# Kernel tuning notes

Measured on AMD Instinct MI355X. Metric: run time of the kernel, lower is better.

The kernel has to match this reference:

```python
import jax, jax.numpy as jnp
import numpy as np

N, E, F_IN, H, OUT, G = 40000, 640000, 128, 128, 10, 256


def setup_inputs() -> dict:
    key = jax.random.key(0)
    ks = jax.random.split(key, 8)
    x = jax.random.normal(ks[0], (N, F_IN), dtype=jnp.float32)
    edge_index = jax.random.randint(ks[1], (2, E), 0, N, dtype=jnp.int32)
    batch = jnp.sort(jax.random.randint(ks[2], (N,), 0, G, dtype=jnp.int32))
    W1 = jax.random.normal(ks[3], (F_IN, H), dtype=jnp.float32) / np.sqrt(F_IN)
    b1 = jnp.zeros((H,), dtype=jnp.float32)
    W2 = jax.random.normal(ks[4], (H, H), dtype=jnp.float32) / np.sqrt(H)
    b2 = jnp.zeros((H,), dtype=jnp.float32)
    Wfc = jax.random.normal(ks[5], (H, OUT), dtype=jnp.float32) / np.sqrt(H)
    bfc = jnp.zeros((OUT,), dtype=jnp.float32)
    return {"x": x, "edge_index": edge_index, "batch": batch,
            "W1": W1, "b1": b1, "W2": W2, "b2": b2, "Wfc": Wfc, "bfc": bfc}


def _gcn_conv(x, W, b, row, col, num_nodes):
    # x' = D^{-1/2} (A+I) D^{-1/2} (x W) + b   (self-loops already in row/col)
    xw = x @ W                                            # [N, H]
    ones = jnp.ones(row.shape[0], dtype=x.dtype)
    deg = jax.ops.segment_sum(ones, col, num_segments=num_nodes)
    dinv = jnp.where(deg > 0, jax.lax.rsqrt(jnp.maximum(deg, 1.0)), 0.0)
    norm = dinv[row] * dinv[col]                          # [E+N]
    msg = xw[row] * norm[:, None]                         # gather + scale
    return jax.ops.segment_sum(msg, col, num_segments=num_nodes) + b


def reference(x, edge_index, batch, W1, b1, W2, b2, Wfc, bfc):
    num_nodes = x.shape[0]
    loop = jnp.arange(num_nodes, dtype=edge_index.dtype)
    row = jnp.concatenate([edge_index[0], loop])
    col = jnp.concatenate([edge_index[1], loop])

    h = jax.nn.relu(_gcn_conv(x, W1, b1, row, col, num_nodes))
    h = jax.nn.relu(_gcn_conv(h, W2, b2, row, col, num_nodes))

    # global_mean_pool over graph ids
    sums = jax.ops.segment_sum(h, batch, num_segments=G)  # [G, H]
    cnt = jax.ops.segment_sum(jnp.ones(num_nodes, h.dtype), batch, num_segments=G)
    pooled = sums / jnp.maximum(cnt, 1.0)[:, None]

    logits = pooled @ Wfc + bfc                           # [G, OUT]
    return jax.nn.log_softmax(logits, axis=-1)
```

## Files before the change

kernel.cpp:

```cpp
#include <hip/hip_runtime.h>
#include <math.h>

#define H_DIM 128
#define OUT_DIM 10

typedef __attribute__((ext_vector_type(8))) __bf16 bf16x8;
typedef __attribute__((ext_vector_type(8))) unsigned short ushort8;
typedef __attribute__((ext_vector_type(4))) float f32x4;

__device__ inline unsigned short f2bf_rne(float f) {
    unsigned int u = __float_as_uint(f);
    unsigned int r = u + 0x7FFFu + ((u >> 16) & 1u);
    return (unsigned short)(r >> 16);
}
__device__ inline float bf_lo(unsigned int u) { return __uint_as_float(u << 16); }
__device__ inline float bf_hi(unsigned int u) { return __uint_as_float(u & 0xFFFF0000u); }

__global__ __launch_bounds__(256) void hist_kernel(const int* __restrict__ col,
                                                   int* __restrict__ cnt, int E) {
    int e = blockIdx.x * 256 + threadIdx.x;
    if (e < E) atomicAdd(&cnt[col[e]], 1);
}

__global__ __launch_bounds__(256) void scan_phase1(const int* __restrict__ cnt,
                                                   int* __restrict__ blockSums,
                                                   float* __restrict__ dinv, int N) {
    __shared__ int red[256];
    int base = blockIdx.x * 1024;
    int t = threadIdx.x;
    int s = 0;
    for (int i = 0; i < 4; ++i) {
        int idx = base + t * 4 + i;
        if (idx < N) {
            int cv = cnt[idx];
            s += cv;
            dinv[idx] = rsqrtf((float)cv + 1.0f);
        }
    }
    red[t] = s;
    __syncthreads();
    for (int d = 128; d > 0; d >>= 1) {
        if (t < d) red[t] += red[t + d];
        __syncthreads();
    }
    if (t == 0) blockSums[blockIdx.x] = red[0];
}

__global__ __launch_bounds__(256) void scan_phase2(const int* __restrict__ blockSums,
                                                   int* __restrict__ blockOffs,
                                                   int* __restrict__ offs, int B, int N) {
    __shared__ int sh[256];
    int t = threadIdx.x;
    sh[t] = (t < B) ? blockSums[t] : 0;
    __syncthreads();
    for (int d = 1; d < 256; d <<= 1) {
        int v = (t >= d) ? sh[t - d] : 0;
        __syncthreads();
        sh[t] += v;
        __syncthreads();
    }
    if (t < B) blockOffs[t] = (t == 0) ? 0 : sh[t - 1];
    if (t == 255) offs[N] = sh[255];
}

__global__ __launch_bounds__(256) void scan_phase3(const int* __restrict__ cnt,
                                                   const int* __restrict__ blockOffs,
                                                   int* __restrict__ offs,
                                                   int* __restrict__ cursor, int N) {
    __shared__ int red[256];
    int base = blockIdx.x * 1024;
    int t = threadIdx.x;
    int v[4];
    int s = 0;
    for (int i = 0; i < 4; ++i) {
        int idx = base + t * 4 + i;
        v[i] = (idx < N) ? cnt[idx] : 0;
        s += v[i];
    }
    red[t] = s;
    __syncthreads();
    for (int d = 1; d < 256; d <<= 1) {
        int x = (t >= d) ? red[t - d] : 0;
        __syncthreads();
        red[t] += x;
        __syncthreads();
    }
    int run = blockOffs[blockIdx.x] + ((t == 0) ? 0 : red[t - 1]);
    for (int i = 0; i < 4; ++i) {
        int idx = base + t * 4 + i;
        if (idx < N) { offs[idx] = run; cursor[idx] = run; run += v[i]; }
    }
}

__global__ __launch_bounds__(256) void scatter_kernel(const int* __restrict__ row,
                                                      const int* __restrict__ col,
                                                      const float* __restrict__ dinv,
                                                      int* __restrict__ cursor,
                                                      int2* __restrict__ csr, int E) {
    int e = blockIdx.x * 256 + threadIdx.x;
    if (e >= E) return;
    int r = row[e], c = col[e];
    int pos = atomicAdd(&cursor[c], 1);
    int2 p; p.x = r; p.y = __float_as_int(dinv[r] * dinv[c]);
    csr[pos] = p;
}

__global__ __launch_bounds__(256) void wconvert(const float* __restrict__ W1,
                                                const float* __restrict__ W2,
                                                unsigned short* __restrict__ Wt1Hi,
                                                unsigned short* __restrict__ Wt1Lo,
                                                unsigned short* __restrict__ Wt2Hi,
                                                unsigned short* __restrict__ Wt2Lo) {
    int i = blockIdx.x * 256 + threadIdx.x;
    const float* src       = (i < 16384) ? W1    : W2;
    unsigned short* dh     = (i < 16384) ? Wt1Hi : Wt2Hi;
    unsigned short* dl     = (i < 16384) ? Wt1Lo : Wt2Lo;
    int idx = i & 16383;
    int k = idx >> 7, n = idx & 127;
    float v = src[idx];
    unsigned short hb = f2bf_rne(v);
    float hf = __uint_as_float((unsigned int)hb << 16);
    unsigned short lb = f2bf_rne(v - hf);
    dh[n * H_DIM + k] = hb;
    dl[n * H_DIM + k] = lb;
}

__global__ __launch_bounds__(256) void xsplit(const float* __restrict__ X,
                                              unsigned short* __restrict__ Xhi,
                                              unsigned short* __restrict__ Xlo,
                                              int total8) {
    int i = blockIdx.x * 256 + threadIdx.x;
    if (i >= total8) return;
    const float* p = X + (size_t)i * 8;
    f32x4 a = *(const f32x4*)p;
    f32x4 b = *(const f32x4*)(p + 4);
    float v[8] = {a.x, a.y, a.z, a.w, b.x, b.y, b.z, b.w};
    ushort8 h, l;
    #pragma unroll
    for (int j = 0; j < 8; ++j) {
        unsigned short hb = f2bf_rne(v[j]);
        float hf = __uint_as_float((unsigned int)hb << 16);
        h[j] = hb;
        l[j] = f2bf_rne(v[j] - hf);
    }
    *(ushort8*)(Xhi + (size_t)i * 8) = h;
    *(ushort8*)(Xlo + (size_t)i * 8) = l;
}

__global__ __launch_bounds__(256) void gemm_mfma_splitA(const unsigned short* __restrict__ Ahi,
                                                        const unsigned short* __restrict__ Alo,
                                                        const unsigned short* __restrict__ WtHi,
                                                        const unsigned short* __restrict__ WtLo,
                                                        unsigned short* __restrict__ Yb, int N) {
    int lane = threadIdx.x & 63;
    int wv   = threadIdx.x >> 6;
    int m16  = lane & 15;
    int quad = lane >> 4;
    int nodeBase = blockIdx.x * 32;

    f32x4 acc[2][2] = {};

    #pragma unroll
    for (int kt = 0; kt < 4; ++kt) {
        int k0 = kt * 32 + quad * 8;

        ushort8 aHi[2], aLo[2];
        #pragma unroll
        for (int mi = 0; mi < 2; ++mi) {
            int node = nodeBase + mi * 16 + m16;
            if (node >= N) node = N - 1;
            size_t off = (size_t)node * H_DIM + k0;
            aHi[mi] = *(const ushort8*)(Ahi + off);
            aLo[mi] = *(const ushort8*)(Alo + off);
        }

        ushort8 bHi[2], bLo[2];
        #pragma unroll
        for (int ni = 0; ni < 2; ++ni) {
            int n = (wv * 2 + ni) * 16 + m16;
            size_t off = (size_t)n * H_DIM + k0;
            bHi[ni] = *(const ushort8*)(WtHi + off);
            bLo[ni] = *(const ushort8*)(WtLo + off);
        }

        #pragma unroll
        for (int mi = 0; mi < 2; ++mi)
            #pragma unroll
            for (int ni = 0; ni < 2; ++ni) {
                acc[mi][ni] = __builtin_amdgcn_mfma_f32_16x16x32_bf16(
                    __builtin_bit_cast(bf16x8, aHi[mi]),
                    __builtin_bit_cast(bf16x8, bHi[ni]), acc[mi][ni], 0, 0, 0);
                acc[mi][ni] = __builtin_amdgcn_mfma_f32_16x16x32_bf16(
                    __builtin_bit_cast(bf16x8, aLo[mi]),
                    __builtin_bit_cast(bf16x8, bHi[ni]), acc[mi][ni], 0, 0, 0);
                acc[mi][ni] = __builtin_amdgcn_mfma_f32_16x16x32_bf16(
                    __builtin_bit_cast(bf16x8, aHi[mi]),
                    __builtin_bit_cast(bf16x8, bLo[ni]), acc[mi][ni], 0, 0, 0);
            }
    }

    #pragma unroll
    for (int mi = 0; mi < 2; ++mi)
        #pragma unroll
        for (int r = 0; r < 4; ++r) {
            int node = nodeBase + mi * 16 + quad * 4 + r;
            if (node < N) {
                #pragma unroll
                for (int ni = 0; ni < 2; ++ni) {
                    int c = (wv * 2 + ni) * 16 + m16;
                    Yb[(size_t)node * H_DIM + c] = f2bf_rne(acc[mi][ni][r]);
                }
            }
        }
}

__global__ __launch_bounds__(256) void gemm_mfma_bf16A(const unsigned short* __restrict__ Xb,
                                                       const unsigned short* __restrict__ WtHi,
                                                       const unsigned short* __restrict__ WtLo,
                                                       unsigned short* __restrict__ Yb, int N) {
    int lane = threadIdx.x & 63;
    int wv   = threadIdx.x >> 6;
    int m16  = lane & 15;
    int quad = lane >> 4;
    int nodeBase = blockIdx.x * 32;

    f32x4 acc[2][2] = {};

    #pragma unroll
    for (int kt = 0; kt < 4; ++kt) {
        int k0 = kt * 32 + quad * 8;

        ushort8 a[2];
        #pragma unroll
        for (int mi = 0; mi < 2; ++mi) {
            int node = nodeBase + mi * 16 + m16;
            if (node >= N) node = N - 1;
            a[mi] = *(const ushort8*)(Xb + (size_t)node * H_DIM + k0);
        }

        ushort8 bHi[2], bLo[2];
        #pragma unroll
        for (int ni = 0; ni < 2; ++ni) {
            int n = (wv * 2 + ni) * 16 + m16;
            size_t off = (size_t)n * H_DIM + k0;
            bHi[ni] = *(const ushort8*)(WtHi + off);
            bLo[ni] = *(const ushort8*)(WtLo + off);
        }

        #pragma unroll
        for (int mi = 0; mi < 2; ++mi)
            #pragma unroll
            for (int ni = 0; ni < 2; ++ni) {
                acc[mi][ni] = __builtin_amdgcn_mfma_f32_16x16x32_bf16(
                    __builtin_bit_cast(bf16x8, a[mi]),
                    __builtin_bit_cast(bf16x8, bHi[ni]), acc[mi][ni], 0, 0, 0);
                acc[mi][ni] = __builtin_amdgcn_mfma_f32_16x16x32_bf16(
                    __builtin_bit_cast(bf16x8, a[mi]),
                    __builtin_bit_cast(bf16x8, bLo[ni]), acc[mi][ni], 0, 0, 0);
            }
    }

    #pragma unroll
    for (int mi = 0; mi < 2; ++mi)
        #pragma unroll
        for (int r = 0; r < 4; ++r) {
            int node = nodeBase + mi * 16 + quad * 4 + r;
            if (node < N) {
                #pragma unroll
                for (int ni = 0; ni < 2; ++ni) {
                    int c = (wv * 2 + ni) * 16 + m16;
                    Yb[(size_t)node * H_DIM + c] = f2bf_rne(acc[mi][ni][r]);
                }
            }
        }
}

__global__ __launch_bounds__(256) void agg_fused(const unsigned short* __restrict__ XWb,
                                                 const float* __restrict__ dinv,
                                                 const int2* __restrict__ csr,
                                                 const int* __restrict__ offs,
                                                 const float* __restrict__ bias,
                                                 unsigned short* __restrict__ OUTb, int N) {
    int wave = (blockIdx.x * 256 + threadIdx.x) >> 6;
    int lane = threadIdx.x & 63;
    if (wave >= N) return;
    int c = wave;
    int start = offs[c], end = offs[c + 1];
    float dc = dinv[c];
    const unsigned int* XW32 = (const unsigned int*)XWb;

    float ax0, ay0;
    {
        unsigned int u = XW32[(size_t)c * 64 + lane];
        float s = dc * dc;
        ax0 = bf_lo(u) * s; ay0 = bf_hi(u) * s;
    }
    float ax1 = 0.f, ay1 = 0.f, ax2 = 0.f, ay2 = 0.f, ax3 = 0.f, ay3 = 0.f;

    for (int base = start; base < end; base += 64) {
        int m = end - base; if (m > 64) m = 64;
        int2 ce; ce.x = 0; ce.y = 0;
        if (lane < m) ce = csr[base + lane];

        int j = 0;
        for (; j + 3 < m; j += 4) {
            int r0 = __shfl(ce.x, j);     int b0 = __shfl(ce.y, j);
            int r1 = __shfl(ce.x, j + 1); int b1 = __shfl(ce.y, j + 1);
            int r2 = __shfl(ce.x, j + 2); int b2 = __shfl(ce.y, j + 2);
            int r3 = __shfl(ce.x, j + 3); int b3 = __shfl(ce.y, j + 3);
            unsigned int g0 = XW32[(size_t)r0 * 64 + lane];
            unsigned int g1 = XW32[(size_t)r1 * 64 + lane];
            unsigned int g2 = XW32[(size_t)r2 * 64 + lane];
            unsigned int g3 = XW32[(size_t)r3 * 64 + lane];
            float n0 = __int_as_float(b0);
            float n1 = __int_as_float(b1);
            float n2 = __int_as_float(b2);
            float n3 = __int_as_float(b3);
            ax0 += bf_lo(g0) * n0; ay0 += bf_hi(g0) * n0;
            ax1 += bf_lo(g1) * n1; ay1 += bf_hi(g1) * n1;
            ax2 += bf_lo(g2) * n2; ay2 += bf_hi(g2) * n2;
            ax3 += bf_lo(g3) * n3; ay3 += bf_hi(g3) * n3;
        }
        for (; j < m; ++j) {
            int r = __shfl(ce.x, j); int b = __shfl(ce.y, j);
            unsigned int g = XW32[(size_t)r * 64 + lane];
            float nrm = __int_as_float(b);
            ax1 += bf_lo(g) * nrm; ay1 += bf_hi(g) * nrm;
        }
    }
    float ax = (ax0 + ax1) + (ax2 + ax3);
    float ay = (ay0 + ay1) + (ay2 + ay3);
    float2 b = ((const float2*)bias)[lane];
    ax = fmaxf(ax + b.x, 0.f);
    ay = fmaxf(ay + b.y, 0.f);
    unsigned int o = (unsigned int)f2bf_rne(ax) | ((unsigned int)f2bf_rne(ay) << 16);
    ((unsigned int*)(OUTb + (size_t)c * H_DIM))[lane] = o;
}

__global__ __launch_bounds__(256) void pool_partial(const unsigned short* __restrict__ Hb,
                                                    const int* __restrict__ batch,
                                                    float* __restrict__ pooledSum, int N) {
    __shared__ int sb[64];
    int base = blockIdx.x * 64;
    int t = threadIdx.x;
    if (t < 64) {
        int idx = base + t;
        sb[t] = (idx < N) ? batch[idx] : -1;
    }
    __syncthreads();
    int f   = t & 127;
    int sub = t >> 7;
    int n0  = sub * 32;
    float acc = 0.f;
    int curg = -1;
    #pragma unroll 4
    for (int i = 0; i < 32; ++i) {
        int n = base + n0 + i;
        if (n >= N) break;
        int g = sb[n0 + i];
        if (g != curg) {
            if (curg >= 0) atomicAdd(&pooledSum[curg * H_DIM + f], acc);
            acc = 0.f; curg = g;
        }
        acc += __uint_as_float(((unsigned int)Hb[(size_t)n * H_DIM + f]) << 16);
    }
    if (curg >= 0) atomicAdd(&pooledSum[curg * H_DIM + f], acc);
}

__global__ __launch_bounds__(64) void head_kernel(const float* __restrict__ pooledSum,
                                                  const int* __restrict__ batch,
                                                  const float* __restrict__ Wfc,
                                                  const float* __restrict__ bfc,
                                                  float* __restrict__ out, int N) {
    __shared__ float sl[OUT_DIM + 2];
    __shared__ int bounds[2];
    int g = blockIdx.x;
    int j = threadIdx.x;
    if (j < 2) {
        int v = g + j;
        int lo = 0, hi = N;
        while (lo < hi) {
            int mid = (lo + hi) >> 1;
            if (batch[mid] < v) lo = mid + 1; else hi = mid;
        }
        bounds[j] = lo;
    }
    __syncthreads();
    int cnt = bounds[1] - bounds[0];
    float inv = 1.0f / (float)(cnt > 0 ? cnt : 1);
    if (j < OUT_DIM) {
        float acc = 0.f;
        const float* p = pooledSum + g * H_DIM;
        for (int k = 0; k < H_DIM; ++k) acc += p[k] * Wfc[k * OUT_DIM + j];
        sl[j] = acc * inv + bfc[j];
    }
    __syncthreads();
    if (j == 0) {
        float m = sl[0];
        for (int i = 1; i < OUT_DIM; ++i) m = fmaxf(m, sl[i]);
        float s = 0.f;
        for (int i = 0; i < OUT_DIM; ++i) s += expf(sl[i] - m);
        sl[OUT_DIM] = m + logf(s);
    }
    __syncthreads();
    if (j < OUT_DIM) out[g * OUT_DIM + j] = sl[j] - sl[OUT_DIM];
}

extern "C" void kernel_launch(void* const* d_in, const int* in_sizes, int n_in,
                              void* d_out, int out_size, void* d_ws, size_t ws_size,
                              hipStream_t stream) {
    const float* x     = (const float*)d_in[0];
    const int*   ei    = (const int*)  d_in[1];
    const int*   batch = (const int*)  d_in[2];
    const float* W1    = (const float*)d_in[3];
    const float* b1    = (const float*)d_in[4];
    const float* W2    = (const float*)d_in[5];
    const float* b2    = (const float*)d_in[6];
    const float* Wfc   = (const float*)d_in[7];
    const float* bfc   = (const float*)d_in[8];
    float* out = (float*)d_out;

    int N = in_sizes[2];
    int E = in_sizes[1] / 2;
    int G = out_size / OUT_DIM;
    const int* row = ei;
    const int* col = ei + E;

    char* wsb = (char*)d_ws;
    size_t nAlign = (size_t)((N + 256) / 256) * 256;
    int*   cnt    = (int*)wsb;
    int*   offs   = cnt + nAlign;
    int*   cursor = offs + nAlign;
    float* dinv   = (float*)(cursor + nAlign);
    int2*  csr    = (int2*)(dinv + nAlign);
    unsigned short* Xb = (unsigned short*)(csr + E);
    unsigned short* Hb = Xb + (size_t)N * H_DIM;
    float* pooledSum = (float*)(Hb + (size_t)N * H_DIM);
    int* blockSums = (int*)(pooledSum + (size_t)G * H_DIM);
    int* blockOffs = blockSums + 256;
    unsigned short* Wt1Hi = (unsigned short*)(blockOffs + 256);
    unsigned short* Wt1Lo = Wt1Hi + H_DIM * H_DIM;
    unsigned short* Wt2Hi = Wt1Lo + H_DIM * H_DIM;
    unsigned short* Wt2Lo = Wt2Hi + H_DIM * H_DIM;
    unsigned short* Xhi = Wt2Lo + H_DIM * H_DIM;
    unsigned short* Xlo = Xhi + (size_t)N * H_DIM;

    int scanBlocks = (N + 1023) / 1024;
    int total8 = N * H_DIM / 8;

    wconvert<<<128, 256, 0, stream>>>(W1, W2, Wt1Hi, Wt1Lo, Wt2Hi, Wt2Lo);
    xsplit<<<(total8 + 255) / 256, 256, 0, stream>>>(x, Xhi, Xlo, total8);

    hipMemsetAsync(cnt, 0, N * sizeof(int), stream);
    hist_kernel<<<(E + 255) / 256, 256, 0, stream>>>(col, cnt, E);
    scan_phase1<<<scanBlocks, 256, 0, stream>>>(cnt, blockSums, dinv, N);
    scan_phase2<<<1, 256, 0, stream>>>(blockSums, blockOffs, offs, scanBlocks, N);
    scan_phase3<<<scanBlocks, 256, 0, stream>>>(cnt, blockOffs, offs, cursor, N);
    scatter_kernel<<<(E + 255) / 256, 256, 0, stream>>>(row, col, dinv, cursor, csr, E);

    int aggBlocks  = (N + 3) / 4;
    int gemmBlocks = (N + 31) / 32;

    gemm_mfma_splitA<<<gemmBlocks, 256, 0, stream>>>(Xhi, Xlo, Wt1Hi, Wt1Lo, Xb, N);
    agg_fused<<<aggBlocks, 256, 0, stream>>>(Xb, dinv, csr, offs, b1, Hb, N);

    gemm_mfma_bf16A<<<gemmBlocks, 256, 0, stream>>>(Hb, Wt2Hi, Wt2Lo, Xb, N);
    agg_fused<<<aggBlocks, 256, 0, stream>>>(Xb, dinv, csr, offs, b2, Hb, N);

    hipMemsetAsync(pooledSum, 0, (size_t)G * H_DIM * sizeof(float), stream);
    pool_partial<<<(N + 63) / 64, 256, 0, stream>>>(Hb, batch, pooledSum, N);
    head_kernel<<<G, 64, 0, stream>>>(pooledSum, batch, Wfc, bfc, out, N);
}
```

Measured before the change: 273.6 us.

## Merge prep kernels and memsets, widen aggregation unroll to eight gathers

Fuses the weight-convert and x-split kernels into one launch selected by block index. Places pooledSum right after cnt so a single memset clears both, which drops one memset call. Raises the aggregation inner-loop unroll from 4 to 8 independent gathers with 8 accumulator pairs, to get more memory-level parallelism on the edge gathers. The costs are higher register pressure in agg_fused and a longer scalar tail loop for low-degree nodes.

New measurement: 278.7 us. No clear change (+1.9%).

```diff
diff --git a/kernel.cpp b/kernel.cpp
--- a/kernel.cpp
+++ b/kernel.cpp
@@ -105,46 +105,47 @@
     csr[pos] = p;
 }
 
-__global__ __launch_bounds__(256) void wconvert(const float* __restrict__ W1,
-                                                const float* __restrict__ W2,
-                                                unsigned short* __restrict__ Wt1Hi,
-                                                unsigned short* __restrict__ Wt1Lo,
-                                                unsigned short* __restrict__ Wt2Hi,
-                                                unsigned short* __restrict__ Wt2Lo) {
-    int i = blockIdx.x * 256 + threadIdx.x;
-    const float* src       = (i < 16384) ? W1    : W2;
-    unsigned short* dh     = (i < 16384) ? Wt1Hi : Wt2Hi;
-    unsigned short* dl     = (i < 16384) ? Wt1Lo : Wt2Lo;
-    int idx = i & 16383;
-    int k = idx >> 7, n = idx & 127;
-    float v = src[idx];
-    unsigned short hb = f2bf_rne(v);
-    float hf = __uint_as_float((unsigned int)hb << 16);
-    unsigned short lb = f2bf_rne(v - hf);
-    dh[n * H_DIM + k] = hb;
-    dl[n * H_DIM + k] = lb;
-}
-
-__global__ __launch_bounds__(256) void xsplit(const float* __restrict__ X,
-                                              unsigned short* __restrict__ Xhi,
-                                              unsigned short* __restrict__ Xlo,
-                                              int total8) {
-    int i = blockIdx.x * 256 + threadIdx.x;
-    if (i >= total8) return;
-    const float* p = X + (size_t)i * 8;
-    f32x4 a = *(const f32x4*)p;
-    f32x4 b = *(const f32x4*)(p + 4);
-    float v[8] = {a.x, a.y, a.z, a.w, b.x, b.y, b.z, b.w};
-    ushort8 h, l;
-    #pragma unroll
-    for (int j = 0; j < 8; ++j) {
-        unsigned short hb = f2bf_rne(v[j]);
+__global__ __launch_bounds__(256) void prep_kernel(const float* __restrict__ W1,
+                                                   const float* __restrict__ W2,
+                                                   unsigned short* __restrict__ Wt1Hi,
+                                                   unsigned short* __restrict__ Wt1Lo,
+                                                   unsigned short* __restrict__ Wt2Hi,
+                                                   unsigned short* __restrict__ Wt2Lo,
+                                                   const float* __restrict__ X,
+                                                   unsigned short* __restrict__ Xhi,
+                                                   unsigned short* __restrict__ Xlo,
+                                                   int total8) {
+    if (blockIdx.x < 128) {
+        int i = blockIdx.x * 256 + threadIdx.x;
+        const float* src   = (i < 16384) ? W1    : W2;
+        unsigned short* dh = (i < 16384) ? Wt1Hi : Wt2Hi;
+        unsigned short* dl = (i < 16384) ? Wt1Lo : Wt2Lo;
+        int idx = i & 16383;
+        int k = idx >> 7, n = idx & 127;
+        float v = src[idx];
+        unsigned short hb = f2bf_rne(v);
         float hf = __uint_as_float((unsigned int)hb << 16);
-        h[j] = hb;
-        l[j] = f2bf_rne(v[j] - hf);
-    }
-    *(ushort8*)(Xhi + (size_t)i * 8) = h;
-    *(ushort8*)(Xlo + (size_t)i * 8) = l;
+        unsigned short lb = f2bf_rne(v - hf);
+        dh[n * H_DIM + k] = hb;
+        dl[n * H_DIM + k] = lb;
+    } else {
+        int i = (blockIdx.x - 128) * 256 + threadIdx.x;
+        if (i >= total8) return;
+        const float* p = X + (size_t)i * 8;
+        f32x4 a = *(const f32x4*)p;
+        f32x4 b = *(const f32x4*)(p + 4);
+        float v[8] = {a.x, a.y, a.z, a.w, b.x, b.y, b.z, b.w};
+        ushort8 h, l;
+        #pragma unroll
+        for (int j = 0; j < 8; ++j) {
+            unsigned short hb = f2bf_rne(v[j]);
+            float hf = __uint_as_float((unsigned int)hb << 16);
+            h[j] = hb;
+            l[j] = f2bf_rne(v[j] - hf);
+        }
+        *(ushort8*)(Xhi + (size_t)i * 8) = h;
+        *(ushort8*)(Xlo + (size_t)i * 8) = l;
+    }
 }
 
 __global__ __launch_bounds__(256) void gemm_mfma_splitA(const unsigned short* __restrict__ Ahi,
@@ -289,13 +290,14 @@
     float dc = dinv[c];
     const unsigned int* XW32 = (const unsigned int*)XWb;
 
-    float ax0, ay0;
+    float ax[8], ay[8];
+    #pragma unroll
+    for (int q = 0; q < 8; ++q) { ax[q] = 0.f; ay[q] = 0.f; }
     {
         unsigned int u = XW32[(size_t)c * 64 + lane];
         float s = dc * dc;
-        ax0 = bf_lo(u) * s; ay0 = bf_hi(u) * s;
-    }
-    float ax1 = 0.f, ay1 = 0.f, ax2 = 0.f, ay2 = 0.f, ax3 = 0.f, ay3 = 0.f;
+        ax[0] = bf_lo(u) * s; ay[0] = bf_hi(u) * s;
+    }
 
     for (int base = start; base < end; base += 64) {
         int m = end - base; if (m > 64) m = 64;
@@ -303,37 +305,36 @@
         if (lane < m) ce = csr[base + lane];
 
         int j = 0;
-        for (; j + 3 < m; j += 4) {
-            int r0 = __shfl(ce.x, j);     int b0 = __shfl(ce.y, j);
-            int r1 = __shfl(ce.x, j + 1); int b1 = __shfl(ce.y, j + 1);
-            int r2 = __shfl(ce.x, j + 2); int b2 = __shfl(ce.y, j + 2);
-            int r3 = __shfl(ce.x, j + 3); int b3 = __shfl(ce.y, j + 3);
-            unsigned int g0 = XW32[(size_t)r0 * 64 + lane];
-            unsigned int g1 = XW32[(size_t)r1 * 64 + lane];
-            unsigned int g2 = XW32[(size_t)r2 * 64 + lane];
-            unsigned int g3 = XW32[(size_t)r3 * 64 + lane];
-            float n0 = __int_as_float(b0);
-            float n1 = __int_as_float(b1);
-            float n2 = __int_as_float(b2);
-            float n3 = __int_as_float(b3);
-            ax0 += bf_lo(g0) * n0; ay0 += bf_hi(g0) * n0;
-            ax1 += bf_lo(g1) * n1; ay1 += bf_hi(g1) * n1;
-            ax2 += bf_lo(g2) * n2; ay2 += bf_hi(g2) * n2;
-            ax3 += bf_lo(g3) * n3; ay3 += bf_hi(g3) * n3;
+        for (; j + 7 < m; j += 8) {
+            int rr[8], bb[8];
+            #pragma unroll
+            for (int q = 0; q < 8; ++q) {
+                rr[q] = __shfl(ce.x, j + q);
+                bb[q] = __shfl(ce.y, j + q);
+            }
+            unsigned int g[8];
+            #pragma unroll
+            for (int q = 0; q < 8; ++q) g[q] = XW32[(size_t)rr[q] * 64 + lane];
+            #pragma unroll
+            for (int q = 0; q < 8; ++q) {
+                float nq = __int_as_float(bb[q]);
+                ax[q] += bf_lo(g[q]) * nq;
+                ay[q] += bf_hi(g[q]) * nq;
+            }
         }
         for (; j < m; ++j) {
             int r = __shfl(ce.x, j); int b = __shfl(ce.y, j);
             unsigned int g = XW32[(size_t)r * 64 + lane];
             float nrm = __int_as_float(b);
-            ax1 += bf_lo(g) * nrm; ay1 += bf_hi(g) * nrm;
-        }
-    }
-    float ax = (ax0 + ax1) + (ax2 + ax3);
-    float ay = (ay0 + ay1) + (ay2 + ay3);
+            ax[1] += bf_lo(g) * nrm; ay[1] += bf_hi(g) * nrm;
+        }
+    }
+    float axs = ((ax[0] + ax[1]) + (ax[2] + ax[3])) + ((ax[4] + ax[5]) + (ax[6] + ax[7]));
+    float ays = ((ay[0] + ay[1]) + (ay[2] + ay[3])) + ((ay[4] + ay[5]) + (ay[6] + ay[7]));
     float2 b = ((const float2*)bias)[lane];
-    ax = fmaxf(ax + b.x, 0.f);
-    ay = fmaxf(ay + b.y, 0.f);
-    unsigned int o = (unsigned int)f2bf_rne(ax) | ((unsigned int)f2bf_rne(ay) << 16);
+    axs = fmaxf(axs + b.x, 0.f);
+    ays = fmaxf(ays + b.y, 0.f);
+    unsigned int o = (unsigned int)f2bf_rne(axs) | ((unsigned int)f2bf_rne(ays) << 16);
     ((unsigned int*)(OUTb + (size_t)c * H_DIM))[lane] = o;
 }
 
@@ -428,15 +429,15 @@
 
     char* wsb = (char*)d_ws;
     size_t nAlign = (size_t)((N + 256) / 256) * 256;
-    int*   cnt    = (int*)wsb;
-    int*   offs   = cnt + nAlign;
-    int*   cursor = offs + nAlign;
-    float* dinv   = (float*)(cursor + nAlign);
-    int2*  csr    = (int2*)(dinv + nAlign);
+    int*   cnt       = (int*)wsb;
+    float* pooledSum = (float*)(cnt + nAlign);
+    int*   offs      = (int*)(pooledSum + (size_t)G * H_DIM);
+    int*   cursor    = offs + nAlign;
+    float* dinv      = (float*)(cursor + nAlign);
+    int2*  csr       = (int2*)(dinv + nAlign);
     unsigned short* Xb = (unsigned short*)(csr + E);
     unsigned short* Hb = Xb + (size_t)N * H_DIM;
-    float* pooledSum = (float*)(Hb + (size_t)N * H_DIM);
-    int* blockSums = (int*)(pooledSum + (size_t)G * H_DIM);
+    int* blockSums = (int*)(Hb + (size_t)N * H_DIM);
     int* blockOffs = blockSums + 256;
     unsigned short* Wt1Hi = (unsigned short*)(blockOffs + 256);
     unsigned short* Wt1Lo = Wt1Hi + H_DIM * H_DIM;
@@ -447,11 +448,13 @@
 
     int scanBlocks = (N + 1023) / 1024;
     int total8 = N * H_DIM / 8;
-
-    wconvert<<<128, 256, 0, stream>>>(W1, W2, Wt1Hi, Wt1Lo, Wt2Hi, Wt2Lo);
-    xsplit<<<(total8 + 255) / 256, 256, 0, stream>>>(x, Xhi, Xlo, total8);
-
-    hipMemsetAsync(cnt, 0, N * sizeof(int), stream);
+    int xsplitBlocks = (total8 + 255) / 256;
+
+    hipMemsetAsync(cnt, 0, (nAlign + (size_t)G * H_DIM) * sizeof(int), stream);
+
+    prep_kernel<<<128 + xsplitBlocks, 256, 0, stream>>>(
+        W1, W2, Wt1Hi, Wt1Lo, Wt2Hi, Wt2Lo, x, Xhi, Xlo, total8);
+
     hist_kernel<<<(E + 255) / 256, 256, 0, stream>>>(col, cnt, E);
     scan_phase1<<<scanBlocks, 256, 0, stream>>>(cnt, blockSums, dinv, N);
     scan_phase2<<<1, 256, 0, stream>>>(blockSums, blockOffs, offs, scanBlocks, N);
@@ -467,7 +470,6 @@
     gemm_mfma_bf16A<<<gemmBlocks, 256, 0, stream>>>(Hb, Wt2Hi, Wt2Lo, Xb, N);
     agg_fused<<<aggBlocks, 256, 0, stream>>>(Xb, dinv, csr, offs, b2, Hb, N);
 
-    hipMemsetAsync(pooledSum, 0, (size_t)G * H_DIM * sizeof(float), stream);
     pool_partial<<<(N + 63) / 64, 256, 0, stream>>>(Hb, batch, pooledSum, N);
     head_kernel<<<G, 64, 0, stream>>>(pooledSum, batch, Wfc, bfc, out, N);
 }
```
